# Performance work log

Hardware: AMD Instinct MI355X
Metric: run time of the kernel (lower is better)

The kernel has to match this reference:

```python
import jax, jax.numpy as jnp
import numpy as np

S = 32
D = S * S          # d = 1024 grid points
DK = 64
R = 4              # heads
NB = 3             # blocks
IN_DIM = 64
EPS = 1e-5
DX = 2.0 / (S - 1)
DXDY = DX * DX
SCALE = 1.0 / np.sqrt(float(DK))


def _edge():
    # grid[i,j] = (gx[i], gx[j]); gridT is the transpose ordering
    gx = jnp.linspace(-1.0, 1.0, S, dtype=jnp.float32)
    g = jnp.stack(jnp.meshgrid(gx, gx, indexing='ij'), axis=-1)  # [S,S,2]
    grid = g.reshape(D, 2)
    gridT = g.transpose(1, 0, 2).reshape(D, 2)
    return jnp.concatenate([
        jnp.broadcast_to(grid[:, None, :], (D, D, 2)),
        jnp.broadcast_to(gridT[None, :, :], (D, D, 2)),
    ], axis=-1)  # [D, D, 4]


def _mlp(e, W1, b1, W2, b2, W3, b3):
    # DenseNet([4,32,64,1], LeakyReLU): two hidden LeakyReLU layers, linear head
    h = jax.nn.leaky_relu(e @ W1 + b1)
    h = jax.nn.leaky_relu(h @ W2 + b2)
    return h @ W3 + b3


def _ln(v, g, b):
    # LayerNorm over normalized_shape [2d, input_dim] -> reduce last two axes
    m = jnp.mean(v, axis=(1, 2), keepdims=True)
    var = jnp.var(v, axis=(1, 2), keepdims=True)
    return (v - m) * jax.lax.rsqrt(var + EPS) * g + b


def setup_inputs() -> dict:
    key = jax.random.key(0)
    ks = jax.random.split(key, 24)
    f32 = jnp.float32

    def nrm(k, shape, fan):
        return jax.random.normal(k, shape, f32) / np.sqrt(float(fan))

    inp = {
        'x': jax.random.normal(ks[0], (8, D, 1), f32),
        'xy': jax.random.normal(ks[1], (8, 2 * D, IN_DIM), f32),
        'P': jnp.zeros((1,), f32),
        # kernel MLP (edge -> weight)
        'kW1': nrm(ks[2], (4, 32), 4), 'kb1': jnp.zeros((32,), f32),
        'kW2': nrm(ks[3], (32, 64), 32), 'kb2': jnp.zeros((64,), f32),
        'kW3': nrm(ks[4], (64, 1), 64), 'kb3': jnp.zeros((1,), f32),
        # kernelf MLP (edge -> weightf)
        'fW1': nrm(ks[5], (4, 32), 4), 'fb1': jnp.zeros((32,), f32),
        'fW2': nrm(ks[6], (32, 64), 32), 'fb2': jnp.zeros((64,), f32),
        'fW3': nrm(ks[7], (64, 1), 64), 'fb3': jnp.zeros((1,), f32),
        # per-(block, head) Q/K linear layers
        'Wq': nrm(ks[8], (NB, R, IN_DIM, DK), IN_DIM),
        'bq': jnp.zeros((NB, R, DK), f32),
        'Wk': nrm(ks[9], (NB, R, IN_DIM, DK), IN_DIM),
        'bk': jnp.zeros((NB, R, DK), f32),
        # per-block LayerNorm affine params over [2d, input_dim]
        'ln_g': jnp.ones((NB, 2 * D, IN_DIM), f32),
        'ln_b': jnp.zeros((NB, 2 * D, IN_DIM), f32),
    }
    return inp


def _forward(x, xy, P, kW1, kb1, kW2, kb2, kW3, kb3,
             fW1, fb1, fW2, fb2, fW3, fb3, Wq, bq, Wk, bk, ln_g, ln_b):
    edge = _edge()
    weight = _mlp(edge, kW1, kb1, kW2, kb2, kW3, kb3).reshape(D, D)   # shared over batch
    weightf = _mlp(edge, fW1, fb1, fW2, fb2, fW3, fb3).reshape(D, D)

    Vinput = _ln(xy, ln_g[0], ln_b[0])  # [b, 2d, in]

    for j in range(NB - 1):
        mid = jnp.zeros_like(Vinput)
        for i in range(R):
            Q = Vinput @ Wq[j, i] + bq[j, i]  # [b, 2d, dk]
            K = Vinput @ Wk[j, i] + bk[j, i]
            Attn = jnp.einsum('bnk,bmk->bnm', Q, K) * SCALE  # [b, 2d, 2d]
            mid = mid + DXDY * jnp.einsum('bnm,bmi->bni', Attn, Vinput)
        Vinput = _ln(mid, ln_g[j + 1], ln_b[j + 1]) + Vinput

    b = xy.shape[0]
    out = jnp.zeros((b, IN_DIM, D), xy.dtype)
    xy_d = xy[:, :D, :]  # [b, d, in]
    for i in range(R):
        Q = Vinput @ Wq[NB - 1, i] + bq[NB - 1, i]
        K = Vinput @ Wk[NB - 1, i] + bk[NB - 1, i]
        Au = jnp.einsum('bnk,bmk->bnm', Q[:, :D], K[:, :D]) * SCALE  # Attn[:, :d, :d]
        Af = jnp.einsum('bnk,bmk->bnm', Q[:, D:], K[:, :D]) * SCALE  # Attn[:, d:, :d]
        Vu = DXDY * jnp.einsum('bnm,bmi->bin', Au, xy_d)  # [b, in, d]
        Vf = DXDY * jnp.einsum('bnm,bmi->bin', Af, xy_d)
        out = out + DXDY * (Vu @ weight) + DXDY * (Vf @ weightf)
    return out.transpose(0, 2, 1)  # [b, d, in]


def reference(x, xy, P, kW1, kb1, kW2, kb2, kW3, kb3,
              fW1, fb1, fW2, fb2, fW3, fb3, Wq, bq, Wk, bk, ln_g, ln_b):
    return _forward(x, xy, P, kW1, kb1, kW2, kb2, kW3, kb3,
                    fW1, fb1, fW2, fb2, fW3, fb3, Wq, bq, Wk, bk, ln_g, ln_b)
```

## Files before the change

### kernel.cpp

```cpp
#include <hip/hip_runtime.h>

namespace {
constexpr int SD = 1024;
constexpr int TD = 2048;
constexpr int BATCH = 8;
constexpr int RH = 4;
constexpr float EPSc = 1e-5f;
constexpr float DXf = 2.0f / 31.0f;
constexpr float DXDYf = DXf * DXf;
constexpr float SCALEf = 0.125f;
constexpr float CFINAL = DXDYf * DXDYf * SCALEf;

constexpr size_t OFF_V   = 0;
constexpr size_t OFF_MID = OFF_V   + (size_t)BATCH * TD * 64;
constexpr size_t OFF_W   = OFF_MID + (size_t)BATCH * TD * 64;
constexpr size_t OFF_WF  = OFF_W   + (size_t)SD * SD;
constexpr size_t OFF_U1K = OFF_WF  + (size_t)SD * SD;
constexpr size_t OFF_U2K = OFF_U1K + SD * 32;
constexpr size_t OFF_U1F = OFF_U2K + SD * 32;
constexpr size_t OFF_U2F = OFF_U1F + SD * 32;
constexpr size_t OFF_GP  = OFF_U2F + SD * 32;
constexpr size_t OFF_SP  = OFF_GP  + (size_t)BATCH * 32 * 4096;
constexpr size_t OFF_A   = OFF_SP  + BATCH * 32 * 64;
constexpr size_t OFF_RV  = OFF_A   + BATCH * 4096;
constexpr size_t OFF_LNP = OFF_RV  + BATCH * 64;
constexpr size_t OFF_ZU  = OFF_LNP + BATCH * 32 * 2;
constexpr size_t OFF_ZF  = OFF_ZU  + (size_t)SD * 512;
constexpr size_t OFF_W1  = OFF_ZF  + (size_t)SD * 512;
constexpr size_t OFF_CS  = OFF_W1  + SD;
constexpr size_t WS_FLOATS = OFF_CS + 16 * SD;
constexpr size_t LIN_OFF = 50704;
}

typedef __bf16 bf16x8 __attribute__((ext_vector_type(8)));
typedef float f32x4 __attribute__((ext_vector_type(4)));

__device__ __forceinline__ float leaky(float x) { return fmaxf(x, 0.01f * x); }
__device__ __forceinline__ float gxv(int i) { return -1.0f + (2.0f / 31.0f) * (float)i; }
__device__ __forceinline__ ushort f2bf(float x) { union { __bf16 b; ushort u; } v; v.b = (__bf16)x; return v.u; }
__device__ __forceinline__ float bf2f(ushort u) { return __uint_as_float(((uint)u) << 16); }

__global__ __launch_bounds__(256) void k_prep(
    const float* __restrict__ kW1, const float* __restrict__ kb1,
    const float* __restrict__ fW1, const float* __restrict__ fb1,
    float* __restrict__ u1k, float* __restrict__ u2k,
    float* __restrict__ u1f, float* __restrict__ u2f,
    const float* __restrict__ kW2, const float* __restrict__ kW3, const float* __restrict__ kb2,
    const float* __restrict__ fW2, const float* __restrict__ fW3, const float* __restrict__ fb2,
    float* __restrict__ LIN,
    const float* __restrict__ Wq, const float* __restrict__ bq,
    const float* __restrict__ Wk, const float* __restrict__ bk,
    float* __restrict__ Ep, float* __restrict__ fp,
    float* __restrict__ gp, float* __restrict__ cp) {
  __shared__ __align__(16) float Wqs[4096];
  __shared__ float Wks[64 * 65];
  __shared__ float bqs[64], bks[64];
  int blk = blockIdx.x, t = threadIdx.x;
  if (blk < 4) {
    int n = blk * 256 + t;
    float ga = gxv(n >> 5), gb = gxv(n & 31);
    for (int j = 0; j < 32; j++) {
      u1k[n * 32 + j] = ga * kW1[j] + gb * kW1[32 + j] + kb1[j];
      u2k[n * 32 + j] = gb * kW1[64 + j] + ga * kW1[96 + j];
      u1f[n * 32 + j] = ga * fW1[j] + gb * fW1[32 + j] + fb1[j];
      u2f[n * 32 + j] = gb * fW1[64 + j] + ga * fW1[96 + j];
    }
    if (blk < 2 && t < 33) {
      const float* W2 = blk ? fW2 : kW2;
      const float* W3 = blk ? fW3 : kW3;
      const float* b2 = blk ? fb2 : kb2;
      if (t < 32) {
        float s = 0.f;
        for (int o = 0; o < 64; o++) s += W2[t * 64 + o] * W3[o];
        LIN[blk * 32 + t] = s;
      } else {
        float s = 0.f;
        for (int o = 0; o < 64; o++) s += b2[o] * W3[o];
        LIN[64 + blk] = s;
      }
    }
    return;
  }
  int h = blk - 4;
  const float* wqb = Wq + (size_t)h * 4096;
  const float* wkb = Wk + (size_t)h * 4096;
  for (int idx = t; idx < 4096; idx += 256) {
    Wqs[idx] = wqb[idx];
    Wks[(idx >> 6) * 65 + (idx & 63)] = wkb[idx];
  }
  if (t < 64) { bqs[t] = bq[h * 64 + t]; bks[t] = bk[h * 64 + t]; }
  __syncthreads();
  int cpp = t & 63, cb = (t >> 6) * 16;
  float acc[16];
#pragma unroll
  for (int u = 0; u < 16; u++) acc[u] = 0.f;
  for (int k = 0; k < 64; k++) {
    float wkv = Wks[cpp * 65 + k];
#pragma unroll
    for (int u = 0; u < 16; u++) acc[u] += Wqs[(cb + u) * 64 + k] * wkv;
  }
  float* eo = Ep + (size_t)h * 4096;
#pragma unroll
  for (int u = 0; u < 16; u++) eo[(cb + u) * 64 + cpp] = acc[u];
  if (t < 64) {
    float f = 0.f, gg = 0.f;
    for (int k = 0; k < 64; k++) {
      f  += Wqs[t * 64 + k] * bks[k];
      gg += Wks[t * 65 + k] * bqs[k];
    }
    fp[h * 64 + t] = f;
    gp[h * 64 + t] = gg;
    float ca = bqs[t] * bks[t];
    ca += __shfl_xor(ca, 1, 64);
    ca += __shfl_xor(ca, 2, 64);
    ca += __shfl_xor(ca, 4, 64);
    ca += __shfl_xor(ca, 8, 64);
    ca += __shfl_xor(ca, 16, 64);
    ca += __shfl_xor(ca, 32, 64);
    if (t == 0) cp[h] = ca;
  }
}

__global__ __launch_bounds__(256) void k_mlp2(
    const float* __restrict__ u1k, const float* __restrict__ u2k,
    const float* __restrict__ kW2, const float* __restrict__ kb2,
    const float* __restrict__ kW3, const float* __restrict__ kb3,
    const float* __restrict__ u1f, const float* __restrict__ u2f,
    const float* __restrict__ fW2, const float* __restrict__ fb2,
    const float* __restrict__ fW3, const float* __restrict__ fb3,
    const float* __restrict__ LIN,
    ushort* __restrict__ outK, ushort* __restrict__ outF) {
  const int which = blockIdx.y;
  const float* u1 = which ? u1f : u1k;
  const float* u2 = which ? u2f : u2k;
  const float* W2 = which ? fW2 : kW2;
  const float* b2 = which ? fb2 : kb2;
  const float* W3 = which ? fW3 : kW3;
  const float* b3 = which ? fb3 : kb3;
  ushort* out = which ? outF : outK;

  const int t = threadIdx.x;
  const int lane = t & 63, wave = t >> 6;
  const int row = lane & 15, grp = lane >> 4;
  const int n0 = (blockIdx.x >> 1) * 2;
  const int mh = blockIdx.x & 1;

  bf16x8 wfrag[4];
  float4 b2q[4], w3q[4];
#pragma unroll
  for (int tt = 0; tt < 4; tt++) {
#pragma unroll
    for (int i = 0; i < 8; i++) wfrag[tt][i] = (__bf16)W2[(grp * 8 + i) * 64 + tt * 16 + row];
    b2q[tt] = *reinterpret_cast<const float4*>(b2 + tt * 16 + grp * 4);
    w3q[tt] = *reinterpret_cast<const float4*>(W3 + tt * 16 + grp * 4);
  }
  float4 l0 = *reinterpret_cast<const float4*>(LIN + which * 32 + grp * 8);
  float4 l1 = *reinterpret_cast<const float4*>(LIN + which * 32 + grp * 8 + 4);
  float linp[8] = {l0.x, l0.y, l0.z, l0.w, l1.x, l1.y, l1.z, l1.w};
  const float cst = 0.505f * LIN[64 + which] + b3[0];

  float u1j[2][8];
#pragma unroll
  for (int nn = 0; nn < 2; nn++)
#pragma unroll
    for (int i = 0; i < 8; i++) u1j[nn][i] = u1[(n0 + nn) * 32 + grp * 8 + i];

#pragma unroll
  for (int chunk = 0; chunk < 2; chunk++) {
#pragma unroll
    for (int st = 0; st < 4; st++) {
      int mbase = mh * 512 + chunk * 256 + wave * 64 + st * 16;
      int m = mbase + row;
      const float4* u2p = reinterpret_cast<const float4*>(u2 + (size_t)m * 32 + grp * 8);
      float4 ua = u2p[0], ub = u2p[1];
      float hv[8] = {ua.x, ua.y, ua.z, ua.w, ub.x, ub.y, ub.z, ub.w};
#pragma unroll
      for (int nn = 0; nn < 2; nn++) {
        float h1f[8];
#pragma unroll
        for (int i = 0; i < 8; i++) h1f[i] = leaky(u1j[nn][i] + hv[i]);
        float accLin = 0.f;
#pragma unroll
        for (int i = 0; i < 8; i++) accLin = fmaf(linp[i], h1f[i], accLin);
        bf16x8 pfrag;
#pragma unroll
        for (int i = 0; i < 8; i++) pfrag[i] = (__bf16)h1f[i];
        float accAbs = 0.f;
#pragma unroll
        for (int tt = 0; tt < 4; tt++) {
          f32x4 ci = {b2q[tt].x, b2q[tt].y, b2q[tt].z, b2q[tt].w};
          f32x4 c = __builtin_amdgcn_mfma_f32_16x16x32_bf16(wfrag[tt], pfrag, ci, 0, 0, 0);
          accAbs = fmaf(fabsf(c[0]), w3q[tt].x, accAbs);
          accAbs = fmaf(fabsf(c[1]), w3q[tt].y, accAbs);
          accAbs = fmaf(fabsf(c[2]), w3q[tt].z, accAbs);
          accAbs = fmaf(fabsf(c[3]), w3q[tt].w, accAbs);
        }
        float red = fmaf(0.495f, accAbs, 0.505f * accLin);
        red += __shfl_xor(red, 16, 64);
        red += __shfl_xor(red, 32, 64);
        if (grp == 0) out[(size_t)(n0 + nn) * SD + mbase + row] = f2bf(red + cst);
      }
    }
  }
}

__global__ __launch_bounds__(256) void k_cvtTb(const ushort* __restrict__ srcA, const ushort* __restrict__ srcB,
                                               ushort* __restrict__ dstA, ushort* __restrict__ dstB) {
  __shared__ float T[64][65];
  const ushort* src = blockIdx.z ? srcB : srcA;
  ushort* dst = blockIdx.z ? dstB : dstA;
  int t = threadIdx.x;
  int c0 = blockIdx.x * 64, r0 = blockIdx.y * 64;
  int rr = t >> 2, cc = (t & 3) * 16;
  const uint4* s4 = reinterpret_cast<const uint4*>(src + (size_t)(r0 + rr) * 1024 + c0 + cc);
  uint4 q0 = s4[0], q1 = s4[1];
  uint qs[8] = {q0.x, q0.y, q0.z, q0.w, q1.x, q1.y, q1.z, q1.w};
#pragma unroll
  for (int j = 0; j < 8; j++) {
    T[rr][cc + 2 * j]     = bf2f((ushort)(qs[j] & 0xffffu));
    T[rr][cc + 2 * j + 1] = bf2f((ushort)(qs[j] >> 16));
  }
  __syncthreads();
  uint pk[8];
#pragma unroll
  for (int j = 0; j < 8; j++) {
    uint lo = (uint)f2bf(T[cc + 2 * j][rr]);
    uint hi = (uint)f2bf(T[cc + 2 * j + 1][rr]);
    pk[j] = lo | (hi << 16);
  }
  ushort* dp = dst + (size_t)(c0 + rr) * 1024 + r0 + cc;
  uint4* dp4 = reinterpret_cast<uint4*>(dp);
  dp4[0] = make_uint4(pk[0], pk[1], pk[2], pk[3]);
  dp4[1] = make_uint4(pk[4], pk[5], pk[6], pk[7]);
}

__global__ __launch_bounds__(256) void k_colsumT(const ushort* __restrict__ WTW, const ushort* __restrict__ WTF,
                                                 float* __restrict__ w1) {
  int t = threadIdx.x;
  int n = blockIdx.x * 16 + (t >> 4), seg = t & 15;
  const uint4* pa = reinterpret_cast<const uint4*>(WTW + (size_t)n * 1024 + seg * 64);
  const uint4* pf = reinterpret_cast<const uint4*>(WTF + (size_t)n * 1024 + seg * 64);
  float s = 0.f;
#pragma unroll
  for (int q = 0; q < 8; q++) {
    uint4 va = pa[q], vf = pf[q];
    uint u[8] = {va.x, va.y, va.z, va.w, vf.x, vf.y, vf.z, vf.w};
#pragma unroll
    for (int j = 0; j < 8; j++) s += bf2f((ushort)(u[j] & 0xffffu)) + bf2f((ushort)(u[j] >> 16));
  }
  s += __shfl_xor(s, 1, 64);
  s += __shfl_xor(s, 2, 64);
  s += __shfl_xor(s, 4, 64);
  s += __shfl_xor(s, 8, 64);
  if (seg == 0) w1[n] = s;
}

__global__ __launch_bounds__(256) void k_redsum(const float* __restrict__ X, float* __restrict__ part) {
  int b = blockIdx.y, c = blockIdx.x, t = threadIdx.x;
  const float4* X4 = reinterpret_cast<const float4*>(X + (size_t)b * 131072 + (size_t)c * 4096);
  float s = 0.f, q = 0.f;
#pragma unroll
  for (int k = 0; k < 4; k++) {
    float4 v = X4[t + k * 256];
    s += v.x + v.y + v.z + v.w;
    q += v.x * v.x + v.y * v.y + v.z * v.z + v.w * v.w;
  }
  for (int off = 32; off; off >>= 1) { s += __shfl_down(s, off); q += __shfl_down(q, off); }
  __shared__ float ss[4], qq[4];
  int lane = t & 63, wid = t >> 6;
  if (lane == 0) { ss[wid] = s; qq[wid] = q; }
  __syncthreads();
  if (t == 0) {
    part[(size_t)(b * 32 + c) * 2] = ss[0] + ss[1] + ss[2] + ss[3];
    part[(size_t)(b * 32 + c) * 2 + 1] = qq[0] + qq[1] + qq[2] + qq[3];
  }
}

__global__ __launch_bounds__(256) void k_apply0(
    const float* __restrict__ src, const float* __restrict__ g,
    const float* __restrict__ bb, const float* __restrict__ lnp,
    float* __restrict__ Vout, float* __restrict__ Gp, float* __restrict__ sp) {
  int c = blockIdx.x, b = blockIdx.y, t = threadIdx.x;
  __shared__ float sm[2];
  __shared__ __align__(16) float Vs[4096];
  if (t == 0) {
    float s = 0.f, q = 0.f;
    for (int cc = 0; cc < 32; cc++) {
      s += lnp[(size_t)(b * 32 + cc) * 2];
      q += lnp[(size_t)(b * 32 + cc) * 2 + 1];
    }
    float mean = s / 131072.0f;
    sm[0] = mean;
    sm[1] = rsqrtf(q / 131072.0f - mean * mean + EPSc);
  }
  __syncthreads();
  float mean = sm[0], is = sm[1];
  size_t base4 = (size_t)b * 32768 + (size_t)c * 1024;
#pragma unroll
  for (int k = 0; k < 4; k++) {
    int idx = t + k * 256;
    float4 v = reinterpret_cast<const float4*>(src)[base4 + idx];
    float4 gg = reinterpret_cast<const float4*>(g)[c * 1024 + idx];
    float4 bv = reinterpret_cast<const float4*>(bb)[c * 1024 + idx];
    float4 r;
    r.x = (v.x - mean) * is * gg.x + bv.x;
    r.y = (v.y - mean) * is * gg.y + bv.y;
    r.z = (v.z - mean) * is * gg.z + bv.z;
    r.w = (v.w - mean) * is * gg.w + bv.w;
    reinterpret_cast<float4*>(Vout)[base4 + idx] = r;
    reinterpret_cast<float4*>(Vs)[idx] = r;
  }
  __syncthreads();
  int tp = t >> 4, tq = t & 15;
  float a2[4][4] = {};
  for (int k = 0; k < 64; k++) {
    float4 xv = *reinterpret_cast<const float4*>(&Vs[k * 64 + tp * 4]);
    float4 yv = *reinterpret_cast<const float4*>(&Vs[k * 64 + tq * 4]);
    a2[0][0] += xv.x * yv.x; a2[0][1] += xv.x * yv.y; a2[0][2] += xv.x * yv.z; a2[0][3] += xv.x * yv.w;
    a2[1][0] += xv.y * yv.x; a2[1][1] += xv.y * yv.y; a2[1][2] += xv.y * yv.z; a2[1][3] += xv.y * yv.w;
    a2[2][0] += xv.z * yv.x; a2[2][1] += xv.z * yv.y; a2[2][2] += xv.z * yv.z; a2[2][3] += xv.z * yv.w;
    a2[3][0] += xv.w * yv.x; a2[3][1] += xv.w * yv.y; a2[3][2] += xv.w * yv.z; a2[3][3] += xv.w * yv.w;
  }
  float* go = Gp + (size_t)(b * 32 + c) * 4096;
#pragma unroll
  for (int i = 0; i < 4; i++) {
    float4 w = {a2[i][0], a2[i][1], a2[i][2], a2[i][3]};
    *reinterpret_cast<float4*>(&go[(tp * 4 + i) * 64 + tq * 4]) = w;
  }
  if (t < 64) {
    float s = 0.f;
    for (int k = 0; k < 64; k++) s += Vs[k * 64 + t];
    sp[(size_t)(b * 32 + c) * 64 + t] = s;
  }
}

__global__ __launch_bounds__(256) void k_gred(const float* __restrict__ Gp, const float* __restrict__ sp,
                                              float* __restrict__ G, float* __restrict__ sv, int nch) {
  int blk = blockIdx.x, b = blockIdx.y, t = threadIdx.x;
  int idx = blk * 256 + t;
  float a = 0.f;
  for (int c = 0; c < nch; c++) a += Gp[(size_t)(b * nch + c) * 4096 + idx];
  G[(size_t)b * 4096 + idx] = a;
  if (blk == 0 && t < 64) {
    float s = 0.f;
    for (int c = 0; c < nch; c++) s += sp[(size_t)(b * nch + c) * 64 + t];
    sv[b * 64 + t] = s;
  }
}

__global__ __launch_bounds__(256) void k_headsA2(
    const float* __restrict__ G, const float* __restrict__ sv,
    const float* __restrict__ Ep, const float* __restrict__ fp,
    const float* __restrict__ gp, const float* __restrict__ cp,
    int j, float scale, int doStats,
    float* __restrict__ A, float* __restrict__ RVo, float* __restrict__ STAT) {
  int b = blockIdx.x, t = threadIdx.x;
  __shared__ float Es[64 * 65];
  __shared__ __align__(16) float Gs[4096];
  __shared__ __align__(16) float As[4096];
  __shared__ float ss[64], fs[64], gs[64];
  __shared__ float cj;
  __shared__ float redbuf[8];
  const float* e0 = Ep + (size_t)(j * RH) * 4096;
  for (int idx = t; idx < 4096; idx += 256) {
    float e = e0[idx] + e0[idx + 4096] + e0[idx + 8192] + e0[idx + 12288];
    Es[(idx >> 6) * 65 + (idx & 63)] = e;
    Gs[idx] = G[(size_t)b * 4096 + idx];
  }
  if (t < 64) {
    ss[t] = sv[b * 64 + t];
    int h0 = j * RH * 64;
    fs[t] = fp[h0 + t] + fp[h0 + 64 + t] + fp[h0 + 128 + t] + fp[h0 + 192 + t];
    gs[t] = gp[h0 + t] + gp[h0 + 64 + t] + gp[h0 + 128 + t] + gp[h0 + 192 + t];
  }
  if (t == 0) cj = cp[j * RH] + cp[j * RH + 1] + cp[j * RH + 2] + cp[j * RH + 3];
  __syncthreads();
  int c = t >> 2, qb = (t & 3) * 16;
  float fv = fs[c];
  float4 acc[4];
#pragma unroll
  for (int u = 0; u < 4; u++) {
    acc[u].x = fv * ss[qb + u * 4 + 0];
    acc[u].y = fv * ss[qb + u * 4 + 1];
    acc[u].z = fv * ss[qb + u * 4 + 2];
    acc[u].w = fv * ss[qb + u * 4 + 3];
  }
  for (int d = 0; d < 64; d++) {
    float ev = Es[c * 65 + d];
    const float4* gr = reinterpret_cast<const float4*>(&Gs[d * 64 + qb]);
#pragma unroll
    for (int u = 0; u < 4; u++) {
      float4 gv = gr[u];
      acc[u].x += ev * gv.x; acc[u].y += ev * gv.y; acc[u].z += ev * gv.z; acc[u].w += ev * gv.w;
    }
  }
  float* ao = A + (size_t)b * 4096 + c * 64 + qb;
#pragma unroll
  for (int u = 0; u < 4; u++) {
    float4 v = acc[u];
    v.x *= scale; v.y *= scale; v.z *= scale; v.w *= scale;
    reinterpret_cast<float4*>(ao)[u] = v;
    *reinterpret_cast<float4*>(&As[c * 64 + qb + u * 4]) = v;
  }
  float rv_t = 0.f;
  if (t < 64) {
    float r = cj * ss[t];
    for (int d = 0; d < 64; d++) r += gs[d] * Gs[d * 64 + t];
    r *= scale;
    RVo[b * 64 + t] = r;
    rv_t = r;
  }
  if (!doStats) return;
  __syncthreads();
  float4 h[4] = {};
  for (int d = 0; d < 64; d++) {
    float gvv = Gs[c * 64 + d];
    const float4* ar = reinterpret_cast<const float4*>(&As[d * 64 + qb]);
#pragma unroll
    for (int u = 0; u < 4; u++) {
      float4 av = ar[u];
      h[u].x += gvv * av.x; h[u].y += gvv * av.y; h[u].z += gvv * av.z; h[u].w += gvv * av.w;
    }
  }
  float tp_ = 0.f;
#pragma unroll
  for (int u = 0; u < 4; u++) {
    float4 a = *reinterpret_cast<const float4*>(&As[c * 64 + qb + u * 4]);
    tp_ += a.x * h[u].x + a.y * h[u].y + a.z * h[u].z + a.w * h[u].w;
  }
  tp_ += __shfl_xor(tp_, 1, 64);  tp_ += __shfl_xor(tp_, 2, 64);
  tp_ += __shfl_xor(tp_, 4, 64);  tp_ += __shfl_xor(tp_, 8, 64);
  tp_ += __shfl_xor(tp_, 16, 64); tp_ += __shfl_xor(tp_, 32, 64);
  if ((t & 63) == 0) redbuf[t >> 6] = tp_;
  if (t < 64) {
    float t1 = 0.f;
    for (int d = 0; d < 64; d++) t1 += ss[d] * As[d * 64 + t];
    float s1 = t1, sr = rv_t, sr2 = rv_t * rv_t, srt = rv_t * t1;
#pragma unroll
    for (int off = 1; off < 64; off <<= 1) {
      s1  += __shfl_xor(s1, off, 64);
      sr  += __shfl_xor(sr, off, 64);
      sr2 += __shfl_xor(sr2, off, 64);
      srt += __shfl_xor(srt, off, 64);
    }
    if (t == 0) { redbuf[4] = s1; redbuf[5] = sr; redbuf[6] = sr2; redbuf[7] = srt; }
  }
  __syncthreads();
  if (t == 0) {
    float tr = redbuf[0] + redbuf[1] + redbuf[2] + redbuf[3];
    float smid = redbuf[4] + 2048.0f * redbuf[5];
    float mu = smid / 131072.0f;
    float e2 = (tr + 2.0f * redbuf[7] + 2048.0f * redbuf[6]) / 131072.0f;
    STAT[b * 2] = mu;
    STAT[b * 2 + 1] = rsqrtf(e2 - mu * mu + EPSc);
  }
}

__global__ __launch_bounds__(256) void k_midapply(
    float* __restrict__ V, const float* __restrict__ A,
    const float* __restrict__ RVv, const float* __restrict__ STAT,
    const float* __restrict__ g, const float* __restrict__ bb,
    const float* __restrict__ Yext,
    float* __restrict__ Gp, float* __restrict__ sp, int nchG) {
  int blk = blockIdx.x, b = blockIdx.y, t = threadIdx.x;
  __shared__ __align__(16) float As[4096];
  __shared__ __align__(16) float Vs[4096];
  __shared__ __align__(16) float Ys[4096];
  __shared__ float rs[64];
  __shared__ float sm[2];
  const float4* A4 = reinterpret_cast<const float4*>(A + (size_t)b * 4096);
#pragma unroll
  for (int k = 0; k < 4; k++) reinterpret_cast<float4*>(As)[t + k * 256] = A4[t + k * 256];
  if (t < 64) rs[t] = RVv[b * 64 + t];
  if (t == 0) { sm[0] = STAT[b * 2]; sm[1] = STAT[b * 2 + 1]; }
  bool doG = (blk < nchG);
  if (Yext != nullptr && doG) {
    size_t yb = (size_t)b * 32768 + (size_t)blk * 1024;
#pragma unroll
    for (int k = 0; k < 4; k++)
      reinterpret_cast<float4*>(Ys)[t + k * 256] = reinterpret_cast<const float4*>(Yext)[yb + t + k * 256];
  }
  __syncthreads();
  float mu = sm[0], is = sm[1];
  int rl = t >> 2, qb = (t & 3) * 16;
  int row = blk * 64 + rl;
  float* vr = V + (size_t)b * 131072 + (size_t)row * 64;
  float4 acc[4];
#pragma unroll
  for (int u = 0; u < 4; u++) {
    acc[u].x = rs[qb + u * 4 + 0]; acc[u].y = rs[qb + u * 4 + 1];
    acc[u].z = rs[qb + u * 4 + 2]; acc[u].w = rs[qb + u * 4 + 3];
  }
  for (int c = 0; c < 64; c++) {
    float vv = vr[c];
    const float4* ar = reinterpret_cast<const float4*>(&As[c * 64 + qb]);
#pragma unroll
    for (int u = 0; u < 4; u++) {
      float4 av = ar[u];
      acc[u].x += vv * av.x; acc[u].y += vv * av.y; acc[u].z += vv * av.z; acc[u].w += vv * av.w;
    }
  }
  const float4* g4 = reinterpret_cast<const float4*>(g + (size_t)row * 64 + qb);
  const float4* b4 = reinterpret_cast<const float4*>(bb + (size_t)row * 64 + qb);
  const float4* vq = reinterpret_cast<const float4*>(vr + qb);
  float4* vo = reinterpret_cast<float4*>(vr + qb);
#pragma unroll
  for (int u = 0; u < 4; u++) {
    float4 gg = g4[u], bv = b4[u], av = vq[u];
    float4 r;
    r.x = (acc[u].x - mu) * is * gg.x + bv.x + av.x;
    r.y = (acc[u].y - mu) * is * gg.y + bv.y + av.y;
    r.z = (acc[u].z - mu) * is * gg.z + bv.z + av.z;
    r.w = (acc[u].w - mu) * is * gg.w + bv.w + av.w;
    vo[u] = r;
    *reinterpret_cast<float4*>(&Vs[rl * 64 + qb + u * 4]) = r;
  }
  __syncthreads();
  if (!doG) return;
  const float* Yp = (Yext != nullptr) ? Ys : Vs;
  int tp = t >> 4, tq = t & 15;
  float a2[4][4] = {};
  for (int k = 0; k < 64; k++) {
    float4 xv = *reinterpret_cast<const float4*>(&Vs[k * 64 + tp * 4]);
    float4 yv = *reinterpret_cast<const float4*>(&Yp[k * 64 + tq * 4]);
    a2[0][0] += xv.x * yv.x; a2[0][1] += xv.x * yv.y; a2[0][2] += xv.x * yv.z; a2[0][3] += xv.x * yv.w;
    a2[1][0] += xv.y * yv.x; a2[1][1] += xv.y * yv.y; a2[1][2] += xv.y * yv.z; a2[1][3] += xv.y * yv.w;
    a2[2][0] += xv.z * yv.x; a2[2][1] += xv.z * yv.y; a2[2][2] += xv.z * yv.z; a2[2][3] += xv.z * yv.w;
    a2[3][0] += xv.w * yv.x; a2[3][1] += xv.w * yv.y; a2[3][2] += xv.w * yv.z; a2[3][3] += xv.w * yv.w;
  }
  float* go = Gp + (size_t)(b * nchG + blk) * 4096;
#pragma unroll
  for (int i = 0; i < 4; i++) {
    float4 w = {a2[i][0], a2[i][1], a2[i][2], a2[i][3]};
    *reinterpret_cast<float4*>(&go[(tp * 4 + i) * 64 + tq * 4]) = w;
  }
  if (t < 64) {
    float s = 0.f;
    for (int k = 0; k < 64; k++) s += Yp[k * 64 + t];
    sp[(size_t)(b * nchG + blk) * 64 + t] = s;
  }
}

__global__ __launch_bounds__(256) void k_y(const float* __restrict__ V, const float* __restrict__ A,
                                           ushort* __restrict__ ZT) {
  int blk = blockIdx.x, b = blockIdx.y, z = blockIdx.z, t = threadIdx.x;
  __shared__ __align__(16) float As[4096];
  __shared__ ushort Zs[64][36];
  const float4* A4 = reinterpret_cast<const float4*>(A + (size_t)b * 4096);
#pragma unroll
  for (int k = 0; k < 4; k++) reinterpret_cast<float4*>(As)[t + k * 256] = A4[t + k * 256];
  __syncthreads();
  int ml = t >> 3, qb = (t & 7) * 8;
  int m = blk * 32 + ml;
  const float* vr = V + (size_t)b * 131072 + (size_t)(z * 1024 + m) * 64;
  float4 acc[2] = {};
  for (int c = 0; c < 64; c++) {
    float vv = vr[c];
    const float4* ar = reinterpret_cast<const float4*>(&As[c * 64 + qb]);
#pragma unroll
    for (int u = 0; u < 2; u++) {
      float4 av = ar[u];
      acc[u].x += vv * av.x; acc[u].y += vv * av.y; acc[u].z += vv * av.z; acc[u].w += vv * av.w;
    }
  }
  Zs[qb + 0][ml] = f2bf(acc[0].x); Zs[qb + 1][ml] = f2bf(acc[0].y);
  Zs[qb + 2][ml] = f2bf(acc[0].z); Zs[qb + 3][ml] = f2bf(acc[0].w);
  Zs[qb + 4][ml] = f2bf(acc[1].x); Zs[qb + 5][ml] = f2bf(acc[1].y);
  Zs[qb + 6][ml] = f2bf(acc[1].z); Zs[qb + 7][ml] = f2bf(acc[1].w);
  __syncthreads();
  int rowq = t >> 2, seg = t & 3;
  const ushort* srcp = &Zs[rowq][seg * 8];
  uint p0 = (uint)srcp[0] | ((uint)srcp[1] << 16);
  uint p1 = (uint)srcp[2] | ((uint)srcp[3] << 16);
  uint p2 = (uint)srcp[4] | ((uint)srcp[5] << 16);
  uint p3 = (uint)srcp[6] | ((uint)srcp[7] << 16);
  ushort* dp = ZT + (size_t)(b * 64 + rowq) * 2048 + (size_t)z * 1024 + blk * 32 + seg * 8;
  *reinterpret_cast<uint4*>(dp) = make_uint4(p0, p1, p2, p3);
}

__global__ __launch_bounds__(256) void k_final_mfma(const ushort* __restrict__ WTW,
                                                    const ushort* __restrict__ WTF,
                                                    const ushort* __restrict__ ZT,
                                                    float* __restrict__ P0, float* __restrict__ P1,
                                                    float* __restrict__ P2, float* __restrict__ P3) {
  int tn = blockIdx.x, tb = blockIdx.y, kz = blockIdx.z, t = threadIdx.x;
  int lane = t & 63, w = t >> 6;
  int wn = w & 1, wb = w >> 1;
  int r = lane & 15, g = lane >> 4;
  int nrow = tn * 32 + wn * 16 + r;
  int bi0 = tb * 64 + wb * 32 + r;
  const ushort* wbase = (kz < 2) ? WTW : WTF;
  const ushort* wp = wbase + (size_t)nrow * 1024 + (kz & 1) * 512 + g * 8;
  const ushort* zp0 = ZT + (size_t)bi0 * 2048 + kz * 512 + g * 8;
  const ushort* zp1 = zp0 + 16 * 2048;
  f32x4 a0 = {0.f, 0.f, 0.f, 0.f}, a1 = a0;
#pragma unroll 4
  for (int ks = 0; ks < 512; ks += 32) {
    bf16x8 fa  = *reinterpret_cast<const bf16x8*>(wp + ks);
    bf16x8 fb0 = *reinterpret_cast<const bf16x8*>(zp0 + ks);
    bf16x8 fb1 = *reinterpret_cast<const bf16x8*>(zp1 + ks);
    a0 = __builtin_amdgcn_mfma_f32_16x16x32_bf16(fa, fb0, a0, 0, 0, 0);
    a1 = __builtin_amdgcn_mfma_f32_16x16x32_bf16(fa, fb1, a1, 0, 0, 0);
  }
  float* P = kz == 0 ? P0 : kz == 1 ? P1 : kz == 2 ? P2 : P3;
  int nbase = tn * 32 + wn * 16 + g * 4;
  int bib = tb * 64 + wb * 32 + r;
#pragma unroll
  for (int rr = 0; rr < 4; rr++) {
    P[(size_t)(nbase + rr) * 512 + bib]      = a0[rr];
    P[(size_t)(nbase + rr) * 512 + bib + 16] = a1[rr];
  }
}

__global__ __launch_bounds__(256) void k_final_red(const float* __restrict__ P0, const float* __restrict__ P1,
                                                   const float* __restrict__ P2, const float* __restrict__ P3,
                                                   const float* __restrict__ w1,
                                                   const float* __restrict__ RV, float* __restrict__ out) {
  int idx4 = blockIdx.x * 256 + threadIdx.x;
  int i4p = idx4 & 15;
  int n = (idx4 >> 4) & 1023;
  int b = idx4 >> 14;
  int pidx = n * 128 + b * 16 + i4p;
  float4 a0 = reinterpret_cast<const float4*>(P0)[pidx];
  float4 a1 = reinterpret_cast<const float4*>(P1)[pidx];
  float4 a2 = reinterpret_cast<const float4*>(P2)[pidx];
  float4 a3 = reinterpret_cast<const float4*>(P3)[pidx];
  float4 d = reinterpret_cast<const float4*>(RV + (size_t)b * 64)[i4p];
  float wv = w1[n];
  float4 r;
  r.x = CFINAL * (a0.x + a1.x + a2.x + a3.x + wv * d.x);
  r.y = CFINAL * (a0.y + a1.y + a2.y + a3.y + wv * d.y);
  r.z = CFINAL * (a0.z + a1.z + a2.z + a3.z + wv * d.z);
  r.w = CFINAL * (a0.w + a1.w + a2.w + a3.w + wv * d.w);
  reinterpret_cast<float4*>(out)[idx4] = r;
}

extern "C" void kernel_launch(void* const* d_in, const int* in_sizes, int n_in,
                              void* d_out, int out_size, void* d_ws, size_t ws_size,
                              hipStream_t stream) {
  (void)in_sizes; (void)n_in; (void)out_size;
  const float* xy  = (const float*)d_in[1];
  const float* kW1 = (const float*)d_in[3];
  const float* kb1 = (const float*)d_in[4];
  const float* kW2 = (const float*)d_in[5];
  const float* kb2 = (const float*)d_in[6];
  const float* kW3 = (const float*)d_in[7];
  const float* kb3 = (const float*)d_in[8];
  const float* fW1 = (const float*)d_in[9];
  const float* fb1 = (const float*)d_in[10];
  const float* fW2 = (const float*)d_in[11];
  const float* fb2 = (const float*)d_in[12];
  const float* fW3 = (const float*)d_in[13];
  const float* fb3 = (const float*)d_in[14];
  const float* Wq  = (const float*)d_in[15];
  const float* bq  = (const float*)d_in[16];
  const float* Wk  = (const float*)d_in[17];
  const float* bk  = (const float*)d_in[18];
  const float* lng = (const float*)d_in[19];
  const float* lnb = (const float*)d_in[20];
  float* ws = (float*)d_ws;
  float* out = (float*)d_out;
  if (ws_size < WS_FLOATS * sizeof(float)) return;

  float* V   = ws + OFF_V;
  float* U1K = ws + OFF_U1K;
  float* U2K = ws + OFF_U2K;
  float* U1F = ws + OFF_U1F;
  float* U2F = ws + OFF_U2F;
  float* GPb = ws + OFF_GP;
  float* SPb = ws + OFF_SP;
  float* LNP = ws + OFF_LNP;
  float* W1v = ws + OFF_W1;
  float* G    = ws + OFF_U1K;
  float* SV   = ws + OFF_U1F;
  float* A    = ws + OFF_A;
  float* RV   = ws + OFF_RV;
  float* STAT = ws + OFF_LNP;
  ushort* Wbf  = (ushort*)(ws + OFF_W);
  ushort* WTW  = (ushort*)(ws + OFF_W + 524288);
  ushort* Wfbf = (ushort*)(ws + OFF_WF);
  ushort* WTF  = (ushort*)(ws + OFF_WF + 524288);
  ushort* ZT   = (ushort*)(ws + OFF_MID);
  float* Ep   = ws + OFF_ZU;
  float* Fp   = ws + OFF_ZU + 49152;
  float* Gpp  = ws + OFF_ZU + 49920;
  float* Cp   = ws + OFF_ZU + 50688;
  float* LIN  = ws + OFF_ZU + LIN_OFF;
  float* P0   = ws + OFF_GP;
  float* P1   = ws + OFF_GP + 524288;
  float* P2   = ws + OFF_MID + 524288;
  float* P3   = ws + OFF_ZU;

  k_prep<<<dim3(16), dim3(256), 0, stream>>>(kW1, kb1, fW1, fb1, U1K, U2K, U1F, U2F,
                                             kW2, kW3, kb2, fW2, fW3, fb2, LIN,
                                             Wq, bq, Wk, bk, Ep, Fp, Gpp, Cp);
  k_mlp2<<<dim3(1024, 2), dim3(256), 0, stream>>>(U1K, U2K, kW2, kb2, kW3, kb3,
                                                  U1F, U2F, fW2, fb2, fW3, fb3, LIN, Wbf, Wfbf);
  k_cvtTb<<<dim3(16, 16, 2), dim3(256), 0, stream>>>(Wbf, Wfbf, WTW, WTF);
  k_colsumT<<<dim3(64), dim3(256), 0, stream>>>(WTW, WTF, W1v);

  k_redsum<<<dim3(32, 8), dim3(256), 0, stream>>>(xy, LNP);
  k_apply0<<<dim3(32, 8), dim3(256), 0, stream>>>(xy, lng, lnb, LNP, V, GPb, SPb);

  for (int j = 0; j < 2; j++) {
    k_gred<<<dim3(16, 8), dim3(256), 0, stream>>>(GPb, SPb, G, SV, 32);
    k_headsA2<<<dim3(8), dim3(256), 0, stream>>>(G, SV, Ep, Fp, Gpp, Cp, j, DXDYf * SCALEf, 1,
                                                 A, RV, STAT);
    k_midapply<<<dim3(32, 8), dim3(256), 0, stream>>>(
        V, A, RV, STAT, lng + (size_t)(j + 1) * 131072, lnb + (size_t)(j + 1) * 131072,
        (j == 1) ? xy : nullptr, GPb, SPb, (j == 1) ? 16 : 32);
  }
  k_gred<<<dim3(16, 8), dim3(256), 0, stream>>>(GPb, SPb, G, SV, 16);
  k_headsA2<<<dim3(8), dim3(256), 0, stream>>>(G, SV, Ep, Fp, Gpp, Cp, 2, 1.0f, 0, A, RV, STAT);
  k_y<<<dim3(32, 8, 2), dim3(256), 0, stream>>>(V, A, ZT);
  k_final_mfma<<<dim3(32, 8, 4), dim3(256), 0, stream>>>(WTW, WTF, ZT, P0, P1, P2, P3);
  k_final_red<<<dim3(512), dim3(256), 0, stream>>>(P0, P1, P2, P3, W1v, RV, out);
}
```

Before: 191.2 us.

## Fuse prep kernels and drop split-K partials in the final GEMM

The reduction-stats kernel is merged into k_prep as extra blocks, and the transpose is merged with the first LayerNorm-apply into one launch. The final GEMM no longer writes four split-K partial buffers followed by a separate reduction kernel. Each block now loops over all K and computes the weight column sums with an extra MFMA against a ones vector, which removes the colsum kernel too. This cuts launches and partial-buffer traffic, but the final GEMM grid is four times smaller (256 blocks) with a longer serial K loop, so it may use the GPU less fully.

```diff
diff --git a/kernel.cpp b/kernel.cpp
--- a/kernel.cpp
+++ b/kernel.cpp
@@ -51,11 +51,34 @@
     const float* __restrict__ Wq, const float* __restrict__ bq,
     const float* __restrict__ Wk, const float* __restrict__ bk,
     float* __restrict__ Ep, float* __restrict__ fp,
-    float* __restrict__ gp, float* __restrict__ cp) {
+    float* __restrict__ gp, float* __restrict__ cp,
+    const float* __restrict__ xy, float* __restrict__ part) {
   __shared__ __align__(16) float Wqs[4096];
   __shared__ float Wks[64 * 65];
   __shared__ float bqs[64], bks[64];
+  __shared__ float ss4[4], qq4[4];
   int blk = blockIdx.x, t = threadIdx.x;
+  if (blk >= 16) {
+    int idx = blk - 16;
+    int b = idx >> 5, c = idx & 31;
+    const float4* X4 = reinterpret_cast<const float4*>(xy + (size_t)b * 131072 + (size_t)c * 4096);
+    float s = 0.f, q = 0.f;
+#pragma unroll
+    for (int k = 0; k < 4; k++) {
+      float4 v = X4[t + k * 256];
+      s += v.x + v.y + v.z + v.w;
+      q += v.x * v.x + v.y * v.y + v.z * v.z + v.w * v.w;
+    }
+    for (int off = 32; off; off >>= 1) { s += __shfl_down(s, off); q += __shfl_down(q, off); }
+    int lane = t & 63, wid = t >> 6;
+    if (lane == 0) { ss4[wid] = s; qq4[wid] = q; }
+    __syncthreads();
+    if (t == 0) {
+      part[(size_t)(b * 32 + c) * 2] = ss4[0] + ss4[1] + ss4[2] + ss4[3];
+      part[(size_t)(b * 32 + c) * 2 + 1] = qq4[0] + qq4[1] + qq4[2] + qq4[3];
+    }
+    return;
+  }
   if (blk < 4) {
     int n = blk * 256 + t;
     float ga = gxv(n >> 5), gb = gxv(n & 31);
@@ -204,85 +227,46 @@
   }
 }
 
-__global__ __launch_bounds__(256) void k_cvtTb(const ushort* __restrict__ srcA, const ushort* __restrict__ srcB,
-                                               ushort* __restrict__ dstA, ushort* __restrict__ dstB) {
-  __shared__ float T[64][65];
-  const ushort* src = blockIdx.z ? srcB : srcA;
-  ushort* dst = blockIdx.z ? dstB : dstA;
-  int t = threadIdx.x;
-  int c0 = blockIdx.x * 64, r0 = blockIdx.y * 64;
-  int rr = t >> 2, cc = (t & 3) * 16;
-  const uint4* s4 = reinterpret_cast<const uint4*>(src + (size_t)(r0 + rr) * 1024 + c0 + cc);
-  uint4 q0 = s4[0], q1 = s4[1];
-  uint qs[8] = {q0.x, q0.y, q0.z, q0.w, q1.x, q1.y, q1.z, q1.w};
-#pragma unroll
-  for (int j = 0; j < 8; j++) {
-    T[rr][cc + 2 * j]     = bf2f((ushort)(qs[j] & 0xffffu));
-    T[rr][cc + 2 * j + 1] = bf2f((ushort)(qs[j] >> 16));
-  }
-  __syncthreads();
-  uint pk[8];
-#pragma unroll
-  for (int j = 0; j < 8; j++) {
-    uint lo = (uint)f2bf(T[cc + 2 * j][rr]);
-    uint hi = (uint)f2bf(T[cc + 2 * j + 1][rr]);
-    pk[j] = lo | (hi << 16);
-  }
-  ushort* dp = dst + (size_t)(c0 + rr) * 1024 + r0 + cc;
-  uint4* dp4 = reinterpret_cast<uint4*>(dp);
-  dp4[0] = make_uint4(pk[0], pk[1], pk[2], pk[3]);
-  dp4[1] = make_uint4(pk[4], pk[5], pk[6], pk[7]);
-}
-
-__global__ __launch_bounds__(256) void k_colsumT(const ushort* __restrict__ WTW, const ushort* __restrict__ WTF,
-                                                 float* __restrict__ w1) {
-  int t = threadIdx.x;
-  int n = blockIdx.x * 16 + (t >> 4), seg = t & 15;
-  const uint4* pa = reinterpret_cast<const uint4*>(WTW + (size_t)n * 1024 + seg * 64);
-  const uint4* pf = reinterpret_cast<const uint4*>(WTF + (size_t)n * 1024 + seg * 64);
-  float s = 0.f;
-#pragma unroll
-  for (int q = 0; q < 8; q++) {
-    uint4 va = pa[q], vf = pf[q];
-    uint u[8] = {va.x, va.y, va.z, va.w, vf.x, vf.y, vf.z, vf.w};
-#pragma unroll
-    for (int j = 0; j < 8; j++) s += bf2f((ushort)(u[j] & 0xffffu)) + bf2f((ushort)(u[j] >> 16));
-  }
-  s += __shfl_xor(s, 1, 64);
-  s += __shfl_xor(s, 2, 64);
-  s += __shfl_xor(s, 4, 64);
-  s += __shfl_xor(s, 8, 64);
-  if (seg == 0) w1[n] = s;
-}
-
-__global__ __launch_bounds__(256) void k_redsum(const float* __restrict__ X, float* __restrict__ part) {
-  int b = blockIdx.y, c = blockIdx.x, t = threadIdx.x;
-  const float4* X4 = reinterpret_cast<const float4*>(X + (size_t)b * 131072 + (size_t)c * 4096);
-  float s = 0.f, q = 0.f;
-#pragma unroll
-  for (int k = 0; k < 4; k++) {
-    float4 v = X4[t + k * 256];
-    s += v.x + v.y + v.z + v.w;
-    q += v.x * v.x + v.y * v.y + v.z * v.z + v.w * v.w;
-  }
-  for (int off = 32; off; off >>= 1) { s += __shfl_down(s, off); q += __shfl_down(q, off); }
-  __shared__ float ss[4], qq[4];
-  int lane = t & 63, wid = t >> 6;
-  if (lane == 0) { ss[wid] = s; qq[wid] = q; }
-  __syncthreads();
-  if (t == 0) {
-    part[(size_t)(b * 32 + c) * 2] = ss[0] + ss[1] + ss[2] + ss[3];
-    part[(size_t)(b * 32 + c) * 2 + 1] = qq[0] + qq[1] + qq[2] + qq[3];
-  }
-}
-
-__global__ __launch_bounds__(256) void k_apply0(
+__global__ __launch_bounds__(256) void k_cvtapply(
+    const ushort* __restrict__ srcA, const ushort* __restrict__ srcB,
+    ushort* __restrict__ dstA, ushort* __restrict__ dstB,
     const float* __restrict__ src, const float* __restrict__ g,
     const float* __restrict__ bb, const float* __restrict__ lnp,
     float* __restrict__ Vout, float* __restrict__ Gp, float* __restrict__ sp) {
-  int c = blockIdx.x, b = blockIdx.y, t = threadIdx.x;
+  __shared__ float T[64][65];
+  __shared__ __align__(16) float Vs[4096];
   __shared__ float sm[2];
-  __shared__ __align__(16) float Vs[4096];
+  int blk = blockIdx.x, t = threadIdx.x;
+  if (blk < 512) {
+    int bx = blk & 15, by = (blk >> 4) & 15, bz = blk >> 8;
+    const ushort* srcp = bz ? srcB : srcA;
+    ushort* dst = bz ? dstB : dstA;
+    int c0 = bx * 64, r0 = by * 64;
+    int rr = t >> 2, cc = (t & 3) * 16;
+    const uint4* s4 = reinterpret_cast<const uint4*>(srcp + (size_t)(r0 + rr) * 1024 + c0 + cc);
+    uint4 q0 = s4[0], q1 = s4[1];
+    uint qs[8] = {q0.x, q0.y, q0.z, q0.w, q1.x, q1.y, q1.z, q1.w};
+#pragma unroll
+    for (int j = 0; j < 8; j++) {
+      T[rr][cc + 2 * j]     = bf2f((ushort)(qs[j] & 0xffffu));
+      T[rr][cc + 2 * j + 1] = bf2f((ushort)(qs[j] >> 16));
+    }
+    __syncthreads();
+    uint pk[8];
+#pragma unroll
+    for (int j = 0; j < 8; j++) {
+      uint lo = (uint)f2bf(T[cc + 2 * j][rr]);
+      uint hi = (uint)f2bf(T[cc + 2 * j + 1][rr]);
+      pk[j] = lo | (hi << 16);
+    }
+    ushort* dp = dst + (size_t)(c0 + rr) * 1024 + r0 + cc;
+    uint4* dp4 = reinterpret_cast<uint4*>(dp);
+    dp4[0] = make_uint4(pk[0], pk[1], pk[2], pk[3]);
+    dp4[1] = make_uint4(pk[4], pk[5], pk[6], pk[7]);
+    return;
+  }
+  int idx2 = blk - 512;
+  int c = idx2 & 31, b = idx2 >> 5;
   if (t == 0) {
     float s = 0.f, q = 0.f;
     for (int cc = 0; cc < 32; cc++) {
@@ -578,61 +562,47 @@
   *reinterpret_cast<uint4*>(dp) = make_uint4(p0, p1, p2, p3);
 }
 
-__global__ __launch_bounds__(256) void k_final_mfma(const ushort* __restrict__ WTW,
-                                                    const ushort* __restrict__ WTF,
-                                                    const ushort* __restrict__ ZT,
-                                                    float* __restrict__ P0, float* __restrict__ P1,
-                                                    float* __restrict__ P2, float* __restrict__ P3) {
-  int tn = blockIdx.x, tb = blockIdx.y, kz = blockIdx.z, t = threadIdx.x;
+__global__ __launch_bounds__(256) void k_final_mfma2(const ushort* __restrict__ WTW,
+                                                     const ushort* __restrict__ WTF,
+                                                     const ushort* __restrict__ ZT,
+                                                     const float* __restrict__ RV,
+                                                     float* __restrict__ out) {
+  int tn = blockIdx.x, tb = blockIdx.y, t = threadIdx.x;
   int lane = t & 63, w = t >> 6;
   int wn = w & 1, wb = w >> 1;
   int r = lane & 15, g = lane >> 4;
   int nrow = tn * 32 + wn * 16 + r;
   int bi0 = tb * 64 + wb * 32 + r;
-  const ushort* wbase = (kz < 2) ? WTW : WTF;
-  const ushort* wp = wbase + (size_t)nrow * 1024 + (kz & 1) * 512 + g * 8;
-  const ushort* zp0 = ZT + (size_t)bi0 * 2048 + kz * 512 + g * 8;
-  const ushort* zp1 = zp0 + 16 * 2048;
-  f32x4 a0 = {0.f, 0.f, 0.f, 0.f}, a1 = a0;
+  bf16x8 ones;
+#pragma unroll
+  for (int i = 0; i < 8; i++) ones[i] = (__bf16)1.0f;
+  f32x4 a0 = {0.f, 0.f, 0.f, 0.f}, a1 = a0, aw = a0;
+  for (int kz = 0; kz < 4; kz++) {
+    const ushort* wbase = (kz < 2) ? WTW : WTF;
+    const ushort* wp = wbase + (size_t)nrow * 1024 + (kz & 1) * 512 + g * 8;
+    const ushort* zp0 = ZT + (size_t)bi0 * 2048 + kz * 512 + g * 8;
+    const ushort* zp1 = zp0 + 16 * 2048;
 #pragma unroll 4
-  for (int ks = 0; ks < 512; ks += 32) {
-    bf16x8 fa  = *reinterpret_cast<const bf16x8*>(wp + ks);
-    bf16x8 fb0 = *reinterpret_cast<const bf16x8*>(zp0 + ks);
-    bf16x8 fb1 = *reinterpret_cast<const bf16x8*>(zp1 + ks);
-    a0 = __builtin_amdgcn_mfma_f32_16x16x32_bf16(fa, fb0, a0, 0, 0, 0);
-    a1 = __builtin_amdgcn_mfma_f32_16x16x32_bf16(fa, fb1, a1, 0, 0, 0);
-  }
-  float* P = kz == 0 ? P0 : kz == 1 ? P1 : kz == 2 ? P2 : P3;
+    for (int ks = 0; ks < 512; ks += 32) {
+      bf16x8 fa  = *reinterpret_cast<const bf16x8*>(wp + ks);
+      bf16x8 fb0 = *reinterpret_cast<const bf16x8*>(zp0 + ks);
+      bf16x8 fb1 = *reinterpret_cast<const bf16x8*>(zp1 + ks);
+      a0 = __builtin_amdgcn_mfma_f32_16x16x32_bf16(fa, fb0, a0, 0, 0, 0);
+      a1 = __builtin_amdgcn_mfma_f32_16x16x32_bf16(fa, fb1, a1, 0, 0, 0);
+      aw = __builtin_amdgcn_mfma_f32_16x16x32_bf16(fa, ones, aw, 0, 0, 0);
+    }
+  }
   int nbase = tn * 32 + wn * 16 + g * 4;
-  int bib = tb * 64 + wb * 32 + r;
+  int i0 = wb * 32 + r;
+  float rv0 = RV[tb * 64 + i0];
+  float rv1 = RV[tb * 64 + i0 + 16];
+  float* op = out + (size_t)tb * 65536;
 #pragma unroll
   for (int rr = 0; rr < 4; rr++) {
-    P[(size_t)(nbase + rr) * 512 + bib]      = a0[rr];
-    P[(size_t)(nbase + rr) * 512 + bib + 16] = a1[rr];
-  }
-}
-
-__global__ __launch_bounds__(256) void k_final_red(const float* __restrict__ P0, const float* __restrict__ P1,
-                                                   const float* __restrict__ P2, const float* __restrict__ P3,
-                                                   const float* __restrict__ w1,
-                                                   const float* __restrict__ RV, float* __restrict__ out) {
-  int idx4 = blockIdx.x * 256 + threadIdx.x;
-  int i4p = idx4 & 15;
-  int n = (idx4 >> 4) & 1023;
-  int b = idx4 >> 14;
-  int pidx = n * 128 + b * 16 + i4p;
-  float4 a0 = reinterpret_cast<const float4*>(P0)[pidx];
-  float4 a1 = reinterpret_cast<const float4*>(P1)[pidx];
-  float4 a2 = reinterpret_cast<const float4*>(P2)[pidx];
-  float4 a3 = reinterpret_cast<const float4*>(P3)[pidx];
-  float4 d = reinterpret_cast<const float4*>(RV + (size_t)b * 64)[i4p];
-  float wv = w1[n];
-  float4 r;
-  r.x = CFINAL * (a0.x + a1.x + a2.x + a3.x + wv * d.x);
-  r.y = CFINAL * (a0.y + a1.y + a2.y + a3.y + wv * d.y);
-  r.z = CFINAL * (a0.z + a1.z + a2.z + a3.z + wv * d.z);
-  r.w = CFINAL * (a0.w + a1.w + a2.w + a3.w + wv * d.w);
-  reinterpret_cast<float4*>(out)[idx4] = r;
+    float w1v = aw[rr];
+    op[(size_t)(nbase + rr) * 64 + i0]      = CFINAL * (a0[rr] + w1v * rv0);
+    op[(size_t)(nbase + rr) * 64 + i0 + 16] = CFINAL * (a1[rr] + w1v * rv1);
+  }
 }
 
 extern "C" void kernel_launch(void* const* d_in, const int* in_sizes, int n_in,
@@ -670,7 +640,6 @@
   float* GPb = ws + OFF_GP;
   float* SPb = ws + OFF_SP;
   float* LNP = ws + OFF_LNP;
-  float* W1v = ws + OFF_W1;
   float* G    = ws + OFF_U1K;
   float* SV   = ws + OFF_U1F;
   float* A    = ws + OFF_A;
@@ -686,21 +655,15 @@
   float* Gpp  = ws + OFF_ZU + 49920;
   float* Cp   = ws + OFF_ZU + 50688;
   float* LIN  = ws + OFF_ZU + LIN_OFF;
-  float* P0   = ws + OFF_GP;
-  float* P1   = ws + OFF_GP + 524288;
-  float* P2   = ws + OFF_MID + 524288;
-  float* P3   = ws + OFF_ZU;
-
-  k_prep<<<dim3(16), dim3(256), 0, stream>>>(kW1, kb1, fW1, fb1, U1K, U2K, U1F, U2F,
-                                             kW2, kW3, kb2, fW2, fW3, fb2, LIN,
-                                             Wq, bq, Wk, bk, Ep, Fp, Gpp, Cp);
+
+  k_prep<<<dim3(272), dim3(256), 0, stream>>>(kW1, kb1, fW1, fb1, U1K, U2K, U1F, U2F,
+                                              kW2, kW3, kb2, fW2, fW3, fb2, LIN,
+                                              Wq, bq, Wk, bk, Ep, Fp, Gpp, Cp,
+                                              xy, LNP);
   k_mlp2<<<dim3(1024, 2), dim3(256), 0, stream>>>(U1K, U2K, kW2, kb2, kW3, kb3,
                                                   U1F, U2F, fW2, fb2, fW3, fb3, LIN, Wbf, Wfbf);
-  k_cvtTb<<<dim3(16, 16, 2), dim3(256), 0, stream>>>(Wbf, Wfbf, WTW, WTF);
-  k_colsumT<<<dim3(64), dim3(256), 0, stream>>>(WTW, WTF, W1v);
-
-  k_redsum<<<dim3(32, 8), dim3(256), 0, stream>>>(xy, LNP);
-  k_apply0<<<dim3(32, 8), dim3(256), 0, stream>>>(xy, lng, lnb, LNP, V, GPb, SPb);
+  k_cvtapply<<<dim3(768), dim3(256), 0, stream>>>(Wbf, Wfbf, WTW, WTF,
+                                                  xy, lng, lnb, LNP, V, GPb, SPb);
 
   for (int j = 0; j < 2; j++) {
     k_gred<<<dim3(16, 8), dim3(256), 0, stream>>>(GPb, SPb, G, SV, 32);
@@ -713,6 +676,5 @@
   k_gred<<<dim3(16, 8), dim3(256), 0, stream>>>(GPb, SPb, G, SV, 16);
   k_headsA2<<<dim3(8), dim3(256), 0, stream>>>(G, SV, Ep, Fp, Gpp, Cp, 2, 1.0f, 0, A, RV, STAT);
   k_y<<<dim3(32, 8, 2), dim3(256), 0, stream>>>(V, A, ZT);
-  k_final_mfma<<<dim3(32, 8, 4), dim3(256), 0, stream>>>(WTW, WTF, ZT, P0, P1, P2, P3);
-  k_final_red<<<dim3(512), dim3(256), 0, stream>>>(P0, P1, P2, P3, W1v, RV, out);
-}
+  k_final_mfma2<<<dim3(32, 8), dim3(256), 0, stream>>>(WTW, WTF, ZT, RV, out);
+}
```

Result: faster. 181.4 us (-5.1%).
